# Performance work log

Hardware: AMD Instinct MI355X
Metric: run time of the kernel (lower is better)

Reference implementation:

```python
import jax, jax.numpy as jnp
import numpy as np

DIM = 2048
K = 8                 # top_k
M = 16                # max_transients
BIND_FRAC = 0.15
BETA = 0.05
GAMMA = 0.9
LIFETIME = 5
B, T = 64, 256

_iu, _ju = np.triu_indices(K, k=1)   # row-major: matches torch's (ii outer, jj inner) loop order
IU = jnp.asarray(_iu, jnp.int32)
JU = jnp.asarray(_ju, jnp.int32)


def _renorm(s):
    n = jnp.sqrt(jnp.sum(jnp.abs(s) ** 2, axis=-1, keepdims=True))
    return s / jnp.maximum(n, 1e-8)


def setup_inputs() -> dict:
    key = jax.random.key(0)
    ks = jax.random.split(key, 5)
    return {
        "x": jax.random.normal(ks[0], (B, T, DIM), jnp.float32),
        "tape_re": jax.random.normal(ks[1], (DIM,), jnp.float32) / np.sqrt(DIM).astype(np.float32),
        "tape_im": jax.random.normal(ks[2], (DIM,), jnp.float32) / np.sqrt(DIM).astype(np.float32),
        "eta_param": jnp.asarray(0.1, jnp.float32),
        "torque_bias_re": jax.random.normal(ks[3], (DIM,), jnp.float32) * 0.01,
        "torque_bias_im": jax.random.normal(ks[4], (DIM,), jnp.float32) * 0.01,
    }


def _per_batch(h, s, ti, tj, mre, mim, cnt, eta, tbias):
    """One timestep for one batch element. s: [D] complex64, transients: 5 arrays of [M]."""
    c = h * s                               # Hadamard reception
    _, top_idx = jax.lax.top_k(jnp.abs(c), K)
    top_c = c[top_idx]
    tm = jnp.abs(top_c)
    ph = jnp.angle(top_c)
    # co-resonance scores for the K*(K-1)/2 pairs; torch detaches via .item()
    score = jax.lax.stop_gradient(tm[IU] * tm[JU] * jnp.cos(ph[IU] - ph[JU]))
    pos = score > 0
    n_pos = jnp.sum(pos.astype(jnp.int32))
    n_bind = jnp.maximum(1, (n_pos.astype(jnp.float32) * BIND_FRAC).astype(jnp.int32))
    sorted_desc = -jnp.sort(-jnp.where(pos, score, -jnp.inf))
    theta_idx = jnp.minimum(n_bind - 1, jnp.maximum(n_pos - 1, 0))
    theta = sorted_desc[theta_idx]
    bind = (score >= theta) & (n_pos > 0)   # theta>0 so only positive scores pass

    ci = top_idx[IU]
    cj = top_idx[JU]
    prod = s[ci] * s[cj]
    mnew = jax.lax.stop_gradient(BETA * prod / jnp.maximum(jnp.abs(prod), 1e-8))  # torch detaches via .item()

    def step(tr, inp):
        ti, tj, mre, mim, cnt = tr
        ci_p, cj_p, do, mr, mi = inp
        active = cnt > 0
        match = active & (((ti == ci_p) & (tj == cj_p)) | ((ti == cj_p) & (tj == ci_p)))
        has_match = jnp.any(match)
        midx = jnp.argmax(match)
        free = ~active
        has_free = jnp.any(free)
        fidx = jnp.argmax(free)
        refresh = do & has_match
        insert = do & (~has_match) & has_free
        cnt = jnp.where(refresh, cnt.at[midx].set(LIFETIME), cnt)
        ti = jnp.where(insert, ti.at[fidx].set(ci_p), ti)
        tj = jnp.where(insert, tj.at[fidx].set(cj_p), tj)
        mre = jnp.where(insert, mre.at[fidx].set(mr), mre)
        mim = jnp.where(insert, mim.at[fidx].set(mi), mim)
        cnt = jnp.where(insert, cnt.at[fidx].set(LIFETIME), cnt)
        return (ti, tj, mre, mim, cnt), None

    (ti, tj, mre, mim, cnt), _ = jax.lax.scan(
        step, (ti, tj, mre, mim, cnt), (ci, cj, bind, mnew.real, mnew.imag))

    # decay all transients
    mre = mre * GAMMA
    mim = mim * GAMMA
    cnt = cnt - 1
    alive = (cnt > 0) & (jnp.sqrt(mre * mre + mim * mim) > 1e-6)
    cnt = jnp.where(alive, cnt, 0)
    mre = jnp.where(alive, mre, 0.0)
    mim = jnp.where(alive, mim, 0.0)

    # augment state with transients (scatter-add to both endpoints)
    s_re = s.real.at[ti].add(0.1 * mre).at[tj].add(0.1 * mre)
    s_im = s.imag.at[ti].add(0.1 * mim).at[tj].add(0.1 * mim)
    s_aug = jax.lax.complex(s_re, s_im)

    c_aug = h * s_aug
    re_c = c_aug.real
    im_c = c_aug.imag
    res_mask = ((re_c > 1e-6) & (jnp.abs(im_c) < re_c)).astype(jnp.float32)
    tor_mask = ((re_c < -1e-6) | (jnp.abs(im_c) >= jnp.abs(re_c))).astype(jnp.float32)
    orth_mask = 1.0 - res_mask - tor_mask
    update = eta * (c_aug * (1.0 - orth_mask) + tor_mask * tbias)
    s_new = _renorm(s + update)
    return s_new, ti, tj, mre, mim, cnt


def _forward(x, tape_re, tape_im, eta_param, torque_bias_re, torque_bias_im):
    Bb, Tt, D = x.shape
    s0 = _renorm(jax.lax.complex(tape_re, tape_im)[None, :])
    s0 = jnp.broadcast_to(s0, (Bb, D))
    eta = jnp.abs(eta_param)
    tbias = jax.lax.complex(torque_bias_re, torque_bias_im)
    ti0 = jnp.zeros((Bb, M), jnp.int32)
    tj0 = jnp.zeros((Bb, M), jnp.int32)
    mre0 = jnp.zeros((Bb, M), jnp.float32)
    mim0 = jnp.zeros((Bb, M), jnp.float32)
    cnt0 = jnp.zeros((Bb, M), jnp.int32)

    step_b = jax.vmap(_per_batch, in_axes=(0, 0, 0, 0, 0, 0, 0, None, None))

    def time_step(carry, h_t):
        s, ti, tj, mre, mim, cnt = carry
        s, ti, tj, mre, mim, cnt = step_b(h_t, s, ti, tj, mre, mim, cnt, eta, tbias)
        return (s, ti, tj, mre, mim, cnt), jnp.abs(s)

    _, outs = jax.lax.scan(time_step, (s0, ti0, tj0, mre0, mim0, cnt0),
                           jnp.transpose(x, (1, 0, 2)))  # [T,B,D]
    return jnp.transpose(outs, (1, 0, 2))                # [B,T,D]


def reference(x, tape_re, tape_im, eta_param, torque_bias_re, torque_bias_im):
    return _forward(x, tape_re, tape_im, eta_param, torque_bias_re, torque_bias_im)
```

## Files before the change

### kernel.cpp

```cpp
#include <hip/hip_runtime.h>
#include <math.h>

#define DIM_ 2048
#define KTOP 8
#define MSLOT 16
#define TSTEPS 256
#define NB 64
#define NTHREADS 320
#define NWORK 256
#define EPT 8
#define CCAP 128

static_assert(NWORK * EPT == DIM_, "mapping");

#define DPP0(src, ctrl, rm) __builtin_amdgcn_update_dpp(0, (src), (ctrl), (rm), 0xf, true)

__device__ __forceinline__ void ced(double &a, double &b) {
  double mx = fmax(a, b);
  b = fmin(a, b);
  a = mx;
}

template <int CTRL, int RM>
__device__ __forceinline__ void merge_2to4_d(double k[8]) {
  int lo0 = DPP0(__double2loint(k[0]), CTRL, RM);
  int hi0 = DPP0(__double2hiint(k[0]), CTRL, RM);
  int lo1 = DPP0(__double2loint(k[1]), CTRL, RM);
  int hi1 = DPP0(__double2hiint(k[1]), CTRL, RM);
  double b0 = __hiloint2double(hi0, lo0);
  double b1 = __hiloint2double(hi1, lo1);
  double z2 = b1, z3 = b0;
  ced(k[0], z2); ced(k[1], z3);
  ced(k[0], k[1]); ced(z2, z3);
  k[2] = z2; k[3] = z3;
}

template <int CTRL, int RM>
__device__ __forceinline__ void merge_first4(double k[8]) {
  double b[4];
#pragma unroll
  for (int i = 0; i < 4; i++) {
    int lo = DPP0(__double2loint(k[i]), CTRL, RM);
    int hi = DPP0(__double2hiint(k[i]), CTRL, RM);
    b[i] = __hiloint2double(hi, lo);
  }
  k[4] = b[3]; k[5] = b[2]; k[6] = b[1]; k[7] = b[0];
  ced(k[0],k[4]); ced(k[1],k[5]); ced(k[2],k[6]); ced(k[3],k[7]);
  ced(k[0],k[2]); ced(k[1],k[3]); ced(k[4],k[6]); ced(k[5],k[7]);
  ced(k[0],k[1]); ced(k[2],k[3]); ced(k[4],k[5]); ced(k[6],k[7]);
}

template <int CTRL, int RM>
__device__ __forceinline__ void merge_level(double k[8]) {
  double b[8];
#pragma unroll
  for (int i = 0; i < 8; i++) {
    int lo = DPP0(__double2loint(k[i]), CTRL, RM);
    int hi = DPP0(__double2hiint(k[i]), CTRL, RM);
    b[i] = __hiloint2double(hi, lo);
  }
#pragma unroll
  for (int i = 0; i < 8; i++) k[i] = fmax(k[i], b[7 - i]);
  ced(k[0],k[4]); ced(k[1],k[5]); ced(k[2],k[6]); ced(k[3],k[7]);
  ced(k[0],k[2]); ced(k[1],k[3]); ced(k[4],k[6]); ced(k[5],k[7]);
  ced(k[0],k[1]); ced(k[2],k[3]); ced(k[4],k[5]); ced(k[6],k[7]);
}

__device__ __forceinline__ void cedf(float &a, float &b) {
  float mx = fmaxf(a, b);
  b = fminf(a, b);
  a = mx;
}
__device__ __forceinline__ void sort4f(float k[8]) {
  cedf(k[0],k[1]); cedf(k[2],k[3]);
  cedf(k[0],k[2]); cedf(k[1],k[3]);
  cedf(k[1],k[2]);
}
template <int CTRL, int RM>
__device__ __forceinline__ void merge_first4_f32(float k[8]) {
  float b[4];
#pragma unroll
  for (int i = 0; i < 4; i++)
    b[i] = __int_as_float(DPP0(__float_as_int(k[i]), CTRL, RM));
  k[4] = b[3]; k[5] = b[2]; k[6] = b[1]; k[7] = b[0];
  cedf(k[0],k[4]); cedf(k[1],k[5]); cedf(k[2],k[6]); cedf(k[3],k[7]);
  cedf(k[0],k[2]); cedf(k[1],k[3]); cedf(k[4],k[6]); cedf(k[5],k[7]);
  cedf(k[0],k[1]); cedf(k[2],k[3]); cedf(k[4],k[5]); cedf(k[6],k[7]);
}
template <int CTRL, int RM>
__device__ __forceinline__ void merge_level_f32(float k[8]) {
  float b[8];
#pragma unroll
  for (int i = 0; i < 8; i++)
    b[i] = __int_as_float(DPP0(__float_as_int(k[i]), CTRL, RM));
#pragma unroll
  for (int i = 0; i < 8; i++) k[i] = fmaxf(k[i], b[7 - i]);
  cedf(k[0],k[4]); cedf(k[1],k[5]); cedf(k[2],k[6]); cedf(k[3],k[7]);
  cedf(k[0],k[2]); cedf(k[1],k[3]); cedf(k[4],k[6]); cedf(k[5],k[7]);
  cedf(k[0],k[1]); cedf(k[2],k[3]); cedf(k[4],k[5]); cedf(k[6],k[7]);
}

#define FMAX_STAGE(x, ctrl, rm)                                                \
  x = fmaxf(x, __int_as_float(DPP0(__float_as_int(x), ctrl, rm)))
#define FADD_STAGE(x, ctrl, rm)                                                \
  x = x + __int_as_float(DPP0(__float_as_int(x), ctrl, rm))

__device__ __forceinline__ float wave_max_f32(float x) {
  FMAX_STAGE(x, 0x111, 0xf);
  FMAX_STAGE(x, 0x112, 0xf);
  FMAX_STAGE(x, 0x114, 0xf);
  FMAX_STAGE(x, 0x118, 0xf);
  FMAX_STAGE(x, 0x142, 0xa);
  FMAX_STAGE(x, 0x143, 0xc);
  return x;
}
__device__ __forceinline__ float wave_sum_f32(float x) {
  FADD_STAGE(x, 0x111, 0xf);
  FADD_STAGE(x, 0x112, 0xf);
  FADD_STAGE(x, 0x114, 0xf);
  FADD_STAGE(x, 0x118, 0xf);
  FADD_STAGE(x, 0x142, 0xa);
  FADD_STAGE(x, 0x143, 0xc);
  return x;
}
__device__ __forceinline__ int rl63(int v) {
  return __builtin_amdgcn_readlane(v, 63);
}

__global__ void __launch_bounds__(NTHREADS)
me_fused(const float *__restrict__ x, const float *__restrict__ tape_re,
         const float *__restrict__ tape_im, const float *__restrict__ eta_param,
         const float *__restrict__ tbias_re, const float *__restrict__ tbias_im,
         float *__restrict__ out) {
  __shared__ float4 sc4[DIM_];
  __shared__ float2 dxy[DIM_];
  __shared__ float4 lmax4[NWORK / 4];
  __shared__ unsigned long long cand_lds[CCAP];
  __shared__ int ccnt;
  __shared__ float red_sh[4];

  const int tid = threadIdx.x;
  const int lane = tid & 63;
  const int wid = tid >> 6;
  const int wtid = tid - 64;
  const int b = blockIdx.x;

  const float eta = fabsf(eta_param[0]);

  float vre[EPT], vim[EPT], tbre_[EPT], tbim_[EPT];
  float hcur[EPT], hnext[EPT], av[EPT];
  const float *xb = x + (size_t)b * TSTEPS * DIM_;

  if (wid > 0) {
    float acc = 0.f, lm = 0.f;
#pragma unroll
    for (int j = 0; j < EPT; j++) {
      int e = wtid + NWORK * j;
      float a = tape_re[e], c2 = tape_im[e];
      vre[j] = a; vim[j] = c2;
      tbre_[j] = tbias_re[e]; tbim_[j] = tbias_im[e];
      float h = xb[e];
      hcur[j] = h; hnext[j] = h;
      dxy[e] = make_float2(0.f, 0.f);
      acc += a * a + c2 * c2;
      float cr = h * a, ci = h * c2;
      av[j] = sqrtf(cr * cr + ci * ci);
      lm = fmaxf(lm, av[j]);
      sc4[e] = make_float4(h, a, c2, 0.f);
    }
    float ws = wave_sum_f32(acc);
    if (lane == 63) red_sh[wid - 1] = ws;
    ((float *)lmax4)[wtid] = lm;
  }
  if (tid == 0) ccnt = 0;

  int s_ti = 0, s_tj = 0, s_cnt = 0;
  float s_mre = 0.f, s_mim = 0.f;

  float osr[EPT], osi[EPT];

  __syncthreads();

  for (int t = 0; t < TSTEPS; t++) {
    float ivn;
    {
      float tot = (red_sh[0] + red_sh[1]) + (red_sh[2] + red_sh[3]);
      ivn = 1.f / fmaxf(sqrtf(tot), 1e-8f);
    }

    if (wid > 0) {
      if (t + 1 < TSTEPS) {
        const float *xr = xb + (size_t)(t + 1) * DIM_;
#pragma unroll
        for (int j = 0; j < EPT; j++) hnext[j] = xr[wtid + NWORK * j];
      }
      if (t > 0) {
        float *op = out + ((size_t)b * TSTEPS + (t - 1)) * DIM_;
#pragma unroll
        for (int j = 0; j < EPT; j++) {
          float sr = vre[j] * ivn, si = vim[j] * ivn;
          op[wtid + NWORK * j] = sqrtf(sr * sr + si * si);
        }
      }
      float4 q = lmax4[lane];
      float k[8];
      k[0] = q.x; k[1] = q.y; k[2] = q.z; k[3] = q.w;
      k[4] = 0.f; k[5] = 0.f; k[6] = 0.f; k[7] = 0.f;
      sort4f(k);
      merge_first4_f32<0x111, 0xf>(k);
      merge_level_f32<0x112, 0xf>(k);
      merge_level_f32<0x114, 0xf>(k);
      merge_level_f32<0x118, 0xf>(k);
      merge_level_f32<0x142, 0xa>(k);
      merge_level_f32<0x143, 0xc>(k);
      float th = __int_as_float(rl63(__float_as_int(k[7])));
#pragma unroll
      for (int j = 0; j < EPT; j++) {
        if (av[j] >= th) {
          int e = wtid + NWORK * j;
          int slot = atomicAdd(&ccnt, 1);
          if (slot < CCAP)
            cand_lds[slot] = (unsigned long long)__double_as_longlong(
                __hiloint2double(__float_as_int(av[j]), ~e));
        }
      }
#pragma unroll
      for (int j = 0; j < EPT; j++) {
        float sri = vre[j] * ivn, sii2 = vim[j] * ivn;
        osr[j] = sri; osi[j] = sii2;
        float h = hcur[j];
        float car = h * sri, cai = h * sii2;
        bool res = (car > 1e-6f) && (fabsf(cai) < car);
        bool tor = (car < -1e-6f) || (fabsf(cai) >= fabsf(car));
        float m1 = (res || tor) ? 1.f : 0.f;
        float mt = tor ? 1.f : 0.f;
        float ur = eta * (car * m1 + mt * tbre_[j]);
        float ui = eta * (cai * m1 + mt * tbim_[j]);
        vre[j] = sri + ur; vim[j] = sii2 + ui;
      }
    }
    __syncthreads();

    if (wid == 0) {
      int cnt = ccnt;
      if (lane == 0) ccnt = 0;
      if (cnt > CCAP) cnt = CCAP;
      unsigned long long u0 = cand_lds[2 * lane];
      unsigned long long u1 = cand_lds[2 * lane + 1];
      double a = (2 * lane < cnt) ? __longlong_as_double((long long)u0) : 0.0;
      double b2 = (2 * lane + 1 < cnt) ? __longlong_as_double((long long)u1) : 0.0;
      double c[8];
      c[0] = fmax(a, b2); c[1] = fmin(a, b2);
      c[2] = 0.0; c[3] = 0.0; c[4] = 0.0; c[5] = 0.0; c[6] = 0.0; c[7] = 0.0;
      merge_2to4_d<0x111, 0xf>(c);
      merge_first4<0x112, 0xf>(c);
      merge_level<0x114, 0xf>(c);
      merge_level<0x118, 0xf>(c);
      int src = 15;
      if (cnt > 32) { merge_level<0x142, 0xa>(c); src = 31; }
      if (cnt > 64) { merge_level<0x143, 0xc>(c); src = 63; }
      int top[KTOP];
#pragma unroll
      for (int r = 0; r < KTOP; r++)
        top[r] = ~__builtin_amdgcn_readlane(__double2loint(c[r]), src);

      int pi = (lane < 28) ? lane : 27;
      int ii = 0, base = 0;
      if (pi >= 7)  { ii = 1; base = 7;  }
      if (pi >= 13) { ii = 2; base = 13; }
      if (pi >= 18) { ii = 3; base = 18; }
      if (pi >= 22) { ii = 4; base = 22; }
      if (pi >= 25) { ii = 5; base = 25; }
      if (pi >= 27) { ii = 6; base = 27; }
      int jj = ii + 1 + (pi - base);
      int gi = top[0];
      if (ii == 1) gi = top[1];
      if (ii == 2) gi = top[2];
      if (ii == 3) gi = top[3];
      if (ii == 4) gi = top[4];
      if (ii == 5) gi = top[5];
      if (ii == 6) gi = top[6];
      int gj = top[1];
      if (jj == 2) gj = top[2];
      if (jj == 3) gj = top[3];
      if (jj == 4) gj = top[4];
      if (jj == 5) gj = top[5];
      if (jj == 6) gj = top[6];
      if (jj == 7) gj = top[7];

      float4 c4i = sc4[gi], c4j = sc4[gj];
      float sri = c4i.y * ivn, sii2 = c4i.z * ivn;
      float srj = c4j.y * ivn, sij = c4j.z * ivn;
      float cri = c4i.x * sri, cii = c4i.x * sii2;
      float crj = c4j.x * srj, cij = c4j.x * sij;
      float score = cri * crj + cii * cij;
      bool valid = (lane < 28);
      bool pos = valid && (score > 0.f);
      unsigned long long posmask = __ballot(pos);
      int npos = __popcll(posmask);
      float pr = sri * srj - sii2 * sij;
      float pq = sri * sij + sii2 * srj;
      float ap = fmaxf(sqrtf(pr * pr + pq * pq), 1e-8f);
      float mr = (0.05f * pr) / ap, mi = (0.05f * pq) / ap;

      unsigned long long bmask = 0ull;
      if (npos > 0) {
        int nbind = (int)((float)npos * 0.15f);
        if (nbind < 1) nbind = 1;
        float val = pos ? score : -__builtin_inff();
        float th2 = 0.f;
        for (int k2 = 0; k2 < nbind; ++k2) {
          float mx = wave_max_f32(val);
          th2 = __int_as_float(rl63(__float_as_int(mx)));
          if (k2 + 1 < nbind) {
            unsigned long long em = __ballot(val == th2);
            if (lane == (int)__builtin_ctzll(em)) val = -__builtin_inff();
          }
        }
        bool bind = valid && (score >= th2);
        bmask = __ballot(bind);
      }
      while (bmask) {
        int pp = (int)__builtin_ctzll(bmask);
        bmask &= bmask - 1;
        int pci = __builtin_amdgcn_readlane(gi, pp);
        int pcj = __builtin_amdgcn_readlane(gj, pp);
        int pmr = __builtin_amdgcn_readlane(__float_as_int(mr), pp);
        int pmi = __builtin_amdgcn_readlane(__float_as_int(mi), pp);
        bool isslot = (lane < MSLOT);
        bool match = isslot && (s_cnt > 0) &&
                     ((s_ti == pci && s_tj == pcj) ||
                      (s_ti == pcj && s_tj == pci));
        unsigned long long mm = __ballot(match);
        if (mm != 0ull) {
          if (lane == (int)__builtin_ctzll(mm)) s_cnt = 5;
        } else {
          unsigned long long fm = __ballot(isslot && s_cnt <= 0);
          if (fm != 0ull && lane == (int)__builtin_ctzll(fm)) {
            s_ti = pci; s_tj = pcj;
            s_mre = __int_as_float(pmr); s_mim = __int_as_float(pmi);
            s_cnt = 5;
          }
        }
      }
      if (lane < MSLOT) {
        s_mre *= 0.9f; s_mim *= 0.9f; s_cnt -= 1;
        bool alive = (s_cnt > 0) &&
                     (sqrtf(s_mre * s_mre + s_mim * s_mim) > 1e-6f);
        if (!alive) { s_cnt = 0; s_mre = 0.f; s_mim = 0.f; }
        if (s_cnt > 0) {
          atomicAdd(&dxy[s_ti].x, 0.1f * s_mre);
          atomicAdd(&dxy[s_tj].x, 0.1f * s_mre);
          atomicAdd(&dxy[s_ti].y, 0.1f * s_mim);
          atomicAdd(&dxy[s_tj].y, 0.1f * s_mim);
        }
      }
    }
    __syncthreads();

    if (wid > 0) {
      float2 dd[EPT];
#pragma unroll
      for (int j = 0; j < EPT; j++) dd[j] = dxy[wtid + NWORK * j];
      float acc2 = 0.f, lm = 0.f;
#pragma unroll
      for (int j = 0; j < EPT; j++) {
        int e = wtid + NWORK * j;
        if (dd[j].x != 0.f || dd[j].y != 0.f) {
          dxy[e] = make_float2(0.f, 0.f);
          float ar = osr[j] + dd[j].x, ai = osi[j] + dd[j].y;
          float h = hcur[j];
          float car = h * ar, cai = h * ai;
          bool res = (car > 1e-6f) && (fabsf(cai) < car);
          bool tor = (car < -1e-6f) || (fabsf(cai) >= fabsf(car));
          float m1 = (res || tor) ? 1.f : 0.f;
          float mt = tor ? 1.f : 0.f;
          float ur = eta * (car * m1 + mt * tbre_[j]);
          float ui = eta * (cai * m1 + mt * tbim_[j]);
          vre[j] = osr[j] + ur; vim[j] = osi[j] + ui;
        }
        acc2 += vre[j] * vre[j] + vim[j] * vim[j];
        float h = hnext[j];
        hcur[j] = h;
        float cr = h * vre[j], ci = h * vim[j];
        av[j] = sqrtf(cr * cr + ci * ci);
        lm = fmaxf(lm, av[j]);
        sc4[e] = make_float4(h, vre[j], vim[j], 0.f);
      }
      float ws = wave_sum_f32(acc2);
      if (lane == 63) red_sh[wid - 1] = ws;
      ((float *)lmax4)[wtid] = lm;
    }
    __syncthreads();
  }

  if (wid > 0) {
    float tot = (red_sh[0] + red_sh[1]) + (red_sh[2] + red_sh[3]);
    float ivnF = 1.f / fmaxf(sqrtf(tot), 1e-8f);
    float *op = out + ((size_t)b * TSTEPS + (TSTEPS - 1)) * DIM_;
#pragma unroll
    for (int j = 0; j < EPT; j++) {
      float sr = vre[j] * ivnF, si = vim[j] * ivnF;
      op[wtid + NWORK * j] = sqrtf(sr * sr + si * si);
    }
  }
}

extern "C" void kernel_launch(void *const *d_in, const int *in_sizes, int n_in,
                              void *d_out, int out_size, void *d_ws,
                              size_t ws_size, hipStream_t stream) {
  const float *x = (const float *)d_in[0];
  const float *tre = (const float *)d_in[1];
  const float *tim = (const float *)d_in[2];
  const float *eta = (const float *)d_in[3];
  const float *tbre = (const float *)d_in[4];
  const float *tbim = (const float *)d_in[5];
  float *out = (float *)d_out;
  me_fused<<<NB, NTHREADS, 0, stream>>>(x, tre, tim, eta, tbre, tbim, out);
}
```

Measured before the change: 1.253 ms.

## Overlap top-k selection with worker update via LDS flag handshake

Wave 0 now computes the top-k directly from per-thread (value, index) maxima packed as doubles, then publishes the threshold through a release flag. Worker waves do their loads, output stores and state update meanwhile. They spin on the flag and add only extra candidates beyond each thread's own maximum. This removes one __syncthreads per timestep and takes the candidate pass off wave 0's critical path. In exchange it adds spin-wait polling and a second merge when extras exist, and it relies on correct intra-workgroup memory ordering.

```diff
diff --git a/kernel.cpp b/kernel.cpp
--- a/kernel.cpp
+++ b/kernel.cpp
@@ -19,6 +19,12 @@
   double mx = fmax(a, b);
   b = fmin(a, b);
   a = mx;
+}
+
+__device__ __forceinline__ void sort4d(double k[8]) {
+  ced(k[0],k[1]); ced(k[2],k[3]);
+  ced(k[0],k[2]); ced(k[1],k[3]);
+  ced(k[1],k[2]);
 }
 
 template <int CTRL, int RM>
@@ -66,40 +72,6 @@
   ced(k[0],k[1]); ced(k[2],k[3]); ced(k[4],k[5]); ced(k[6],k[7]);
 }
 
-__device__ __forceinline__ void cedf(float &a, float &b) {
-  float mx = fmaxf(a, b);
-  b = fminf(a, b);
-  a = mx;
-}
-__device__ __forceinline__ void sort4f(float k[8]) {
-  cedf(k[0],k[1]); cedf(k[2],k[3]);
-  cedf(k[0],k[2]); cedf(k[1],k[3]);
-  cedf(k[1],k[2]);
-}
-template <int CTRL, int RM>
-__device__ __forceinline__ void merge_first4_f32(float k[8]) {
-  float b[4];
-#pragma unroll
-  for (int i = 0; i < 4; i++)
-    b[i] = __int_as_float(DPP0(__float_as_int(k[i]), CTRL, RM));
-  k[4] = b[3]; k[5] = b[2]; k[6] = b[1]; k[7] = b[0];
-  cedf(k[0],k[4]); cedf(k[1],k[5]); cedf(k[2],k[6]); cedf(k[3],k[7]);
-  cedf(k[0],k[2]); cedf(k[1],k[3]); cedf(k[4],k[6]); cedf(k[5],k[7]);
-  cedf(k[0],k[1]); cedf(k[2],k[3]); cedf(k[4],k[5]); cedf(k[6],k[7]);
-}
-template <int CTRL, int RM>
-__device__ __forceinline__ void merge_level_f32(float k[8]) {
-  float b[8];
-#pragma unroll
-  for (int i = 0; i < 8; i++)
-    b[i] = __int_as_float(DPP0(__float_as_int(k[i]), CTRL, RM));
-#pragma unroll
-  for (int i = 0; i < 8; i++) k[i] = fmaxf(k[i], b[7 - i]);
-  cedf(k[0],k[4]); cedf(k[1],k[5]); cedf(k[2],k[6]); cedf(k[3],k[7]);
-  cedf(k[0],k[2]); cedf(k[1],k[3]); cedf(k[4],k[6]); cedf(k[5],k[7]);
-  cedf(k[0],k[1]); cedf(k[2],k[3]); cedf(k[4],k[5]); cedf(k[6],k[7]);
-}
-
 #define FMAX_STAGE(x, ctrl, rm)                                                \
   x = fmaxf(x, __int_as_float(DPP0(__float_as_int(x), ctrl, rm)))
 #define FADD_STAGE(x, ctrl, rm)                                                \
@@ -134,9 +106,12 @@
          float *__restrict__ out) {
   __shared__ float4 sc4[DIM_];
   __shared__ float2 dxy[DIM_];
-  __shared__ float4 lmax4[NWORK / 4];
+  __shared__ __align__(16) uint2 lmax2[NWORK];
   __shared__ unsigned long long cand_lds[CCAP];
-  __shared__ int ccnt;
+  __shared__ int extra_cnt;
+  __shared__ int theta_flag;
+  __shared__ int extras_done;
+  __shared__ unsigned int theta_hi_sh, theta_lo_sh;
   __shared__ float red_sh[4];
 
   const int tid = threadIdx.x;
@@ -149,10 +124,13 @@
 
   float vre[EPT], vim[EPT], tbre_[EPT], tbim_[EPT];
   float hcur[EPT], hnext[EPT], av[EPT];
+  float osr[EPT], osi[EPT];
+  unsigned int lmlo = 0;
   const float *xb = x + (size_t)b * TSTEPS * DIM_;
 
+  if (tid == 0) { extra_cnt = 0; theta_flag = 0; extras_done = 0; }
   if (wid > 0) {
-    float acc = 0.f, lm = 0.f;
+    float acc = 0.f, lm = -1.f;
 #pragma unroll
     for (int j = 0; j < EPT; j++) {
       int e = wtid + NWORK * j;
@@ -165,19 +143,17 @@
       acc += a * a + c2 * c2;
       float cr = h * a, ci = h * c2;
       av[j] = sqrtf(cr * cr + ci * ci);
-      lm = fmaxf(lm, av[j]);
+      unsigned int lo = ~(unsigned int)e;
+      if (av[j] > lm || (av[j] == lm && lo > lmlo)) { lm = av[j]; lmlo = lo; }
       sc4[e] = make_float4(h, a, c2, 0.f);
     }
     float ws = wave_sum_f32(acc);
     if (lane == 63) red_sh[wid - 1] = ws;
-    ((float *)lmax4)[wtid] = lm;
+    lmax2[wtid] = make_uint2((unsigned int)__float_as_int(lm), lmlo);
   }
-  if (tid == 0) ccnt = 0;
 
   int s_ti = 0, s_tj = 0, s_cnt = 0;
   float s_mre = 0.f, s_mim = 0.f;
-
-  float osr[EPT], osi[EPT];
 
   __syncthreads();
 
@@ -188,81 +164,77 @@
       ivn = 1.f / fmaxf(sqrtf(tot), 1e-8f);
     }
 
-    if (wid > 0) {
-      if (t + 1 < TSTEPS) {
-        const float *xr = xb + (size_t)(t + 1) * DIM_;
-#pragma unroll
-        for (int j = 0; j < EPT; j++) hnext[j] = xr[wtid + NWORK * j];
-      }
-      if (t > 0) {
-        float *op = out + ((size_t)b * TSTEPS + (t - 1)) * DIM_;
-#pragma unroll
-        for (int j = 0; j < EPT; j++) {
-          float sr = vre[j] * ivn, si = vim[j] * ivn;
-          op[wtid + NWORK * j] = sqrtf(sr * sr + si * si);
-        }
-      }
-      float4 q = lmax4[lane];
-      float k[8];
-      k[0] = q.x; k[1] = q.y; k[2] = q.z; k[3] = q.w;
-      k[4] = 0.f; k[5] = 0.f; k[6] = 0.f; k[7] = 0.f;
-      sort4f(k);
-      merge_first4_f32<0x111, 0xf>(k);
-      merge_level_f32<0x112, 0xf>(k);
-      merge_level_f32<0x114, 0xf>(k);
-      merge_level_f32<0x118, 0xf>(k);
-      merge_level_f32<0x142, 0xa>(k);
-      merge_level_f32<0x143, 0xc>(k);
-      float th = __int_as_float(rl63(__float_as_int(k[7])));
-#pragma unroll
-      for (int j = 0; j < EPT; j++) {
-        if (av[j] >= th) {
-          int e = wtid + NWORK * j;
-          int slot = atomicAdd(&ccnt, 1);
-          if (slot < CCAP)
-            cand_lds[slot] = (unsigned long long)__double_as_longlong(
-                __hiloint2double(__float_as_int(av[j]), ~e));
-        }
-      }
-#pragma unroll
-      for (int j = 0; j < EPT; j++) {
-        float sri = vre[j] * ivn, sii2 = vim[j] * ivn;
-        osr[j] = sri; osi[j] = sii2;
-        float h = hcur[j];
-        float car = h * sri, cai = h * sii2;
-        bool res = (car > 1e-6f) && (fabsf(cai) < car);
-        bool tor = (car < -1e-6f) || (fabsf(cai) >= fabsf(car));
-        float m1 = (res || tor) ? 1.f : 0.f;
-        float mt = tor ? 1.f : 0.f;
-        float ur = eta * (car * m1 + mt * tbre_[j]);
-        float ui = eta * (cai * m1 + mt * tbim_[j]);
-        vre[j] = sri + ur; vim[j] = sii2 + ui;
-      }
-    }
-    __syncthreads();
-
     if (wid == 0) {
-      int cnt = ccnt;
-      if (lane == 0) ccnt = 0;
-      if (cnt > CCAP) cnt = CCAP;
-      unsigned long long u0 = cand_lds[2 * lane];
-      unsigned long long u1 = cand_lds[2 * lane + 1];
-      double a = (2 * lane < cnt) ? __longlong_as_double((long long)u0) : 0.0;
-      double b2 = (2 * lane + 1 < cnt) ? __longlong_as_double((long long)u1) : 0.0;
+      uint2 q0 = lmax2[lane * 4 + 0], q1 = lmax2[lane * 4 + 1];
+      uint2 q2 = lmax2[lane * 4 + 2], q3 = lmax2[lane * 4 + 3];
       double c[8];
-      c[0] = fmax(a, b2); c[1] = fmin(a, b2);
-      c[2] = 0.0; c[3] = 0.0; c[4] = 0.0; c[5] = 0.0; c[6] = 0.0; c[7] = 0.0;
-      merge_2to4_d<0x111, 0xf>(c);
-      merge_first4<0x112, 0xf>(c);
+      c[0] = __hiloint2double((int)q0.x, (int)q0.y);
+      c[1] = __hiloint2double((int)q1.x, (int)q1.y);
+      c[2] = __hiloint2double((int)q2.x, (int)q2.y);
+      c[3] = __hiloint2double((int)q3.x, (int)q3.y);
+      c[4] = 0.0; c[5] = 0.0; c[6] = 0.0; c[7] = 0.0;
+      sort4d(c);
+      merge_first4<0x111, 0xf>(c);
+      merge_level<0x112, 0xf>(c);
       merge_level<0x114, 0xf>(c);
       merge_level<0x118, 0xf>(c);
-      int src = 15;
-      if (cnt > 32) { merge_level<0x142, 0xa>(c); src = 31; }
-      if (cnt > 64) { merge_level<0x143, 0xc>(c); src = 63; }
+      merge_level<0x142, 0xa>(c);
+      merge_level<0x143, 0xc>(c);
+      int th_hi = rl63(__double2hiint(c[7]));
+      int th_lo = rl63(__double2loint(c[7]));
+      if (lane == 0) {
+        theta_hi_sh = (unsigned int)th_hi;
+        theta_lo_sh = (unsigned int)th_lo;
+        __hip_atomic_store(&theta_flag, t + 1, __ATOMIC_RELEASE,
+                           __HIP_MEMORY_SCOPE_WORKGROUP);
+      }
+      int toph[KTOP], topl[KTOP];
+#pragma unroll
+      for (int r = 0; r < KTOP; r++) {
+        toph[r] = rl63(__double2hiint(c[r]));
+        topl[r] = rl63(__double2loint(c[r]));
+      }
+      while (__hip_atomic_load(&extras_done, __ATOMIC_ACQUIRE,
+                               __HIP_MEMORY_SCOPE_WORKGROUP) < 4 * (t + 1)) {
+        __builtin_amdgcn_s_sleep(1);
+      }
+      int ec = extra_cnt;
+      if (lane == 0) extra_cnt = 0;
+      if (ec > 0) {
+        int ecc = ec; if (ecc > CCAP - 8) ecc = CCAP - 8;
+        int khi = toph[0], klo = topl[0];
+        if (lane == 1) { khi = toph[1]; klo = topl[1]; }
+        if (lane == 2) { khi = toph[2]; klo = topl[2]; }
+        if (lane == 3) { khi = toph[3]; klo = topl[3]; }
+        if (lane == 4) { khi = toph[4]; klo = topl[4]; }
+        if (lane == 5) { khi = toph[5]; klo = topl[5]; }
+        if (lane == 6) { khi = toph[6]; klo = topl[6]; }
+        if (lane == 7) { khi = toph[7]; klo = topl[7]; }
+        if (lane < 8)
+          cand_lds[lane] = ((unsigned long long)(unsigned int)khi << 32) |
+                           (unsigned int)klo;
+        int cnt = 8 + ecc;
+        unsigned long long u0 = cand_lds[2 * lane];
+        unsigned long long u1 = cand_lds[2 * lane + 1];
+        double a = (2 * lane < cnt) ? __longlong_as_double((long long)u0) : 0.0;
+        double b2 = (2 * lane + 1 < cnt) ? __longlong_as_double((long long)u1) : 0.0;
+        double d[8];
+        d[0] = fmax(a, b2); d[1] = fmin(a, b2);
+        d[2] = 0.0; d[3] = 0.0; d[4] = 0.0; d[5] = 0.0; d[6] = 0.0; d[7] = 0.0;
+        merge_2to4_d<0x111, 0xf>(d);
+        merge_first4<0x112, 0xf>(d);
+        int src = 3;
+        if (cnt > 8)  { merge_level<0x114, 0xf>(d); src = 7;  }
+        if (cnt > 16) { merge_level<0x118, 0xf>(d); src = 15; }
+        if (cnt > 32) { merge_level<0x142, 0xa>(d); src = 31; }
+        if (cnt > 64) { merge_level<0x143, 0xc>(d); src = 63; }
+#pragma unroll
+        for (int r = 0; r < KTOP; r++)
+          topl[r] = __builtin_amdgcn_readlane(__double2loint(d[r]), src);
+      }
       int top[KTOP];
 #pragma unroll
-      for (int r = 0; r < KTOP; r++)
-        top[r] = ~__builtin_amdgcn_readlane(__double2loint(c[r]), src);
+      for (int r = 0; r < KTOP; r++) top[r] = ~topl[r];
 
       int pi = (lane < 28) ? lane : 27;
       int ii = 0, base = 0;
@@ -355,6 +327,55 @@
           atomicAdd(&dxy[s_tj].y, 0.1f * s_mim);
         }
       }
+    } else {
+      if (t + 1 < TSTEPS) {
+        const float *xr = xb + (size_t)(t + 1) * DIM_;
+#pragma unroll
+        for (int j = 0; j < EPT; j++) hnext[j] = xr[wtid + NWORK * j];
+      }
+#pragma unroll
+      for (int j = 0; j < EPT; j++) {
+        osr[j] = vre[j] * ivn; osi[j] = vim[j] * ivn;
+      }
+      if (t > 0) {
+        float *op = out + ((size_t)b * TSTEPS + (t - 1)) * DIM_;
+#pragma unroll
+        for (int j = 0; j < EPT; j++)
+          op[wtid + NWORK * j] = sqrtf(osr[j] * osr[j] + osi[j] * osi[j]);
+      }
+#pragma unroll
+      for (int j = 0; j < EPT; j++) {
+        float sri = osr[j], sii2 = osi[j];
+        float h = hcur[j];
+        float car = h * sri, cai = h * sii2;
+        bool res = (car > 1e-6f) && (fabsf(cai) < car);
+        bool tor = (car < -1e-6f) || (fabsf(cai) >= fabsf(car));
+        float m1 = (res || tor) ? 1.f : 0.f;
+        float mt = tor ? 1.f : 0.f;
+        float ur = eta * (car * m1 + mt * tbre_[j]);
+        float ui = eta * (cai * m1 + mt * tbim_[j]);
+        vre[j] = sri + ur; vim[j] = sii2 + ui;
+      }
+      while (__hip_atomic_load(&theta_flag, __ATOMIC_ACQUIRE,
+                               __HIP_MEMORY_SCOPE_WORKGROUP) < t + 1) {
+        __builtin_amdgcn_s_sleep(1);
+      }
+      unsigned int th_hi = theta_hi_sh, th_lo = theta_lo_sh;
+#pragma unroll
+      for (int j = 0; j < EPT; j++) {
+        unsigned int hb = (unsigned int)__float_as_int(av[j]);
+        unsigned int lo = ~(unsigned int)(wtid + NWORK * j);
+        bool isext = (hb > th_hi) || (hb == th_hi && lo > th_lo);
+        if (isext && lo != lmlo) {
+          int slot = atomicAdd(&extra_cnt, 1);
+          if (8 + slot < CCAP)
+            cand_lds[8 + slot] =
+                ((unsigned long long)hb << 32) | (unsigned long long)lo;
+        }
+      }
+      if (lane == 0)
+        __hip_atomic_fetch_add(&extras_done, 1, __ATOMIC_RELEASE,
+                               __HIP_MEMORY_SCOPE_WORKGROUP);
     }
     __syncthreads();
 
@@ -362,7 +383,8 @@
       float2 dd[EPT];
 #pragma unroll
       for (int j = 0; j < EPT; j++) dd[j] = dxy[wtid + NWORK * j];
-      float acc2 = 0.f, lm = 0.f;
+      float acc2 = 0.f, lm = -1.f;
+      lmlo = 0;
 #pragma unroll
       for (int j = 0; j < EPT; j++) {
         int e = wtid + NWORK * j;
@@ -384,12 +406,13 @@
         hcur[j] = h;
         float cr = h * vre[j], ci = h * vim[j];
         av[j] = sqrtf(cr * cr + ci * ci);
-        lm = fmaxf(lm, av[j]);
+        unsigned int lo = ~(unsigned int)e;
+        if (av[j] > lm || (av[j] == lm && lo > lmlo)) { lm = av[j]; lmlo = lo; }
         sc4[e] = make_float4(h, vre[j], vim[j], 0.f);
       }
       float ws = wave_sum_f32(acc2);
       if (lane == 63) red_sh[wid - 1] = ws;
-      ((float *)lmax4)[wtid] = lm;
+      lmax2[wtid] = make_uint2((unsigned int)__float_as_int(lm), lmlo);
     }
     __syncthreads();
   }
```

Result: slower. 1.347 ms (+7.5%).
